# Optimization experiments

Measured on AMD Instinct MI355X. Metric: run time of the kernel, lower is better.

## Reference

```python
import jax, jax.numpy as jnp
import numpy as np
from jax import lax

EPS = 1e-5  # torch LayerNorm / BatchNorm1d default eps
HEADS, DH, DEPTH, C = 4, 128, 2, 512


def setup_inputs() -> dict:
    key = jax.random.key(0)
    ks = iter(jax.random.split(key, 48))
    def rn(shape, scale=1.0):
        return jax.random.normal(next(ks), shape, jnp.float32) * scale
    d, L = 1024, DEPTH
    inp = {}
    inp['x'] = rn((16, 10, 256, d))                      # (b, ncrops, T, d)
    # Temporal embedding: Conv1d(d -> 512, k=3, pad=1) + ReLU
    inp['W_emb'] = rn((C, d, 3), (d * 3) ** -0.5)
    inp['b_emb'] = jnp.zeros((C,), jnp.float32)
    # Transformer (depth=2), params stacked along layer axis
    inp['ln1_g'] = jnp.ones((L, C), jnp.float32); inp['ln1_b'] = jnp.zeros((L, C), jnp.float32)
    inp['W_qkv'] = rn((L, C, 4 * HEADS * DH), C ** -0.5)  # to_qkv (no bias), inner_dim*4 = 2048
    inp['W_o']  = rn((L, 2 * HEADS * DH, C), (2 * HEADS * DH) ** -0.5)
    inp['b_o']  = jnp.zeros((L, C), jnp.float32)
    inp['ln2_g'] = jnp.ones((L, C), jnp.float32); inp['ln2_b'] = jnp.zeros((L, C), jnp.float32)
    inp['W_f1'] = rn((L, C, C), C ** -0.5); inp['b_f1'] = jnp.zeros((L, C), jnp.float32)
    inp['W_f2'] = rn((L, C, C), C ** -0.5); inp['b_f2'] = jnp.zeros((L, C), jnp.float32)
    # NormalHead: conv1 512->32 (k=1), bn1, conv2 32->16 (k=1), bn2, conv3 16->1 (k=1)
    inp['c1_W'] = rn((32, C), C ** -0.5); inp['c1_b'] = jnp.zeros((32,), jnp.float32)
    inp['bn1_g'] = jnp.ones((32,), jnp.float32); inp['bn1_b'] = jnp.zeros((32,), jnp.float32)
    inp['bn1_m'] = rn((32,), 0.1)
    inp['bn1_v'] = jax.random.uniform(next(ks), (32,), jnp.float32, 0.5, 1.5)
    inp['c2_W'] = rn((16, 32), 32 ** -0.5); inp['c2_b'] = jnp.zeros((16,), jnp.float32)
    inp['bn2_g'] = jnp.ones((16,), jnp.float32); inp['bn2_b'] = jnp.zeros((16,), jnp.float32)
    inp['bn2_m'] = rn((16,), 0.1)
    inp['bn2_v'] = jax.random.uniform(next(ks), (16,), jnp.float32, 0.5, 1.5)
    inp['c3_W'] = rn((1, 16), 0.25); inp['c3_b'] = jnp.zeros((1,), jnp.float32)
    return inp


def _ln(z, g, b):
    m = z.mean(-1, keepdims=True)
    v = ((z - m) ** 2).mean(-1, keepdims=True)
    return (z - m) / jnp.sqrt(v + EPS) * g + b


def _bn_eval(z, g, b, m, v):  # z: (B, C, T), eval-mode BatchNorm1d
    return (z - m[None, :, None]) / jnp.sqrt(v[None, :, None] + EPS) * g[None, :, None] + b[None, :, None]


def _k1conv(z, W, b):  # pointwise Conv1d: z (B, Ci, T), W (Co, Ci)
    return jnp.einsum('bct,oc->bot', z, W) + b[None, :, None]


def reference(x, W_emb, b_emb, ln1_g, ln1_b, W_qkv, W_o, b_o, ln2_g, ln2_b,
              W_f1, b_f1, W_f2, b_f2, c1_W, c1_b, bn1_g, bn1_b, bn1_m, bn1_v,
              c2_W, c2_b, bn2_g, bn2_b, bn2_m, bn2_v, c3_W, c3_b):
    b, n, T, d = x.shape
    h = x.reshape(b * n, T, d)
    # Temporal embedding: Conv1d(k=3, pad=1) + ReLU
    h = lax.conv_general_dilated(h.transpose(0, 2, 1), W_emb, (1,), 'SAME',
                                 dimension_numbers=('NCH', 'OIH', 'NCH'))
    h = jax.nn.relu(h + b_emb[None, :, None]).transpose(0, 2, 1)  # (BN, T, 512)

    # fixed positional-decay attention map attn2 (T, T), batch-independent
    idx = jnp.arange(T, dtype=jnp.float32)
    tg = jnp.abs(idx[None, :] - idx[:, None])
    a2 = jnp.exp(-tg / jnp.exp(1.0))
    a2 = a2 / a2.sum(-1)  # NOTE: broadcast over last axis, exactly as in the torch code

    scale = DH ** -0.5
    for l in range(DEPTH):
        z = _ln(h, ln1_g[l], ln1_b[l])
        qkvt = z @ W_qkv[l]                                   # (BN, T, 2048)
        q, k, v, t = jnp.split(qkvt, 4, axis=-1)
        def to_heads(u):
            return u.reshape(u.shape[0], T, HEADS, DH).transpose(0, 2, 1, 3)
        q, k, v, t = map(to_heads, (q, k, v, t))              # (BN, H, T, DH)
        attn1 = jax.nn.softmax(jnp.einsum('bhid,bhjd->bhij', q, k) * scale, axis=-1)
        o1 = jnp.einsum('bhij,bhjd->bhid', attn1, v)
        o2 = jnp.einsum('ij,bhjd->bhid', a2, t)
        o = jnp.concatenate([o1, o2], axis=-1)                # (BN, H, T, 2*DH)
        o = o.transpose(0, 2, 1, 3).reshape(h.shape[0], T, HEADS * 2 * DH)
        h = o @ W_o[l] + b_o[l] + h                           # attn residual
        z = _ln(h, ln2_g[l], ln2_b[l])
        h = (jax.nn.gelu(z @ W_f1[l] + b_f1[l], approximate=False) @ W_f2[l] + b_f2[l]) + h

    # NormalHead on (BN, C, T)
    f = h.transpose(0, 2, 1)
    x1 = _k1conv(f, c1_W, c1_b)                               # (BN, 32, T)
    x2 = _k1conv(jax.nn.relu(_bn_eval(x1, bn1_g, bn1_b, bn1_m, bn1_v)), c2_W, c2_b)  # (BN, 16, T)
    scores = jax.nn.sigmoid(_k1conv(jax.nn.relu(_bn_eval(x2, bn2_g, bn2_b, bn2_m, bn2_v)), c3_W, c3_b))
    normal_scores = scores.reshape(b, n, T).mean(1)           # mean over ncrops -> (b, T)

    def maha(feats, anchor, var):  # Mahalanobis distance vs BN running stats (no eps, as in source)
        dist = jnp.sqrt(jnp.sum((feats - anchor[None, :, None]) ** 2 / var[None, :, None], axis=1))
        return dist.reshape(b, n, T).mean(1)

    distance_sum = maha(x1, bn1_m, bn1_v) + maha(x2, bn2_m, bn2_v)
    return distance_sum * normal_scores                       # (b, T)
```

## Files before the change

### kernel.cpp

```cpp
#include <hip/hip_runtime.h>
#include <math.h>

#define T_    256
#define D_    1024
#define C_    512
#define H_    4
#define DH_   128
#define BNB   160
#define LEPS  1e-5f
#define INV_E 0.36787944117144233f
#define SCALE_ 0.08838834764831845f
#define LDT   40
#define XROW  264192

typedef unsigned short ushort;
typedef unsigned int   uint;
typedef __attribute__((ext_vector_type(8))) short short8;
typedef __attribute__((ext_vector_type(4))) float f32x4;

__device__ __forceinline__ ushort f2b(float f) {
    uint u = __float_as_uint(f);
    u += 0x7fffu + ((u >> 16) & 1u);
    return (ushort)(u >> 16);
}
__device__ __forceinline__ float b2f(ushort u) {
    return __uint_as_float(((uint)u) << 16);
}
__device__ __forceinline__ uint pk(float a, float b) {
    return (uint)f2b(a) | ((uint)f2b(b) << 16);
}
__device__ __forceinline__ void gl2lds(const void* g, void* l) {
    __builtin_amdgcn_global_load_lds(
        (const __attribute__((address_space(1))) void*)g,
        (__attribute__((address_space(3))) void*)l, 16, 0, 0);
}

__global__ void zero_k(float* __restrict__ p, int n) {
    int i = blockIdx.x * 256 + threadIdx.x;
    if (i < n) p[i] = 0.0f;
}

__global__ void xcvt_k(const float* __restrict__ src, ushort* __restrict__ dst, int n4) {
    int i = blockIdx.x * 256 + threadIdx.x;
    if (i < n4) {
        float4 f = ((const float4*)src)[i];
        uint2 v;
        v.x = pk(f.x, f.y);
        v.y = pk(f.z, f.w);
        int e   = i * 4;
        int bn  = e >> 18;
        int rem = e & 262143;
        ((uint2*)(dst + (size_t)bn * XROW + 1024 + rem))[0] = v;
    }
}

__global__ void xpad_k(ushort* __restrict__ dst, int nbn) {
    int i = blockIdx.x * 256 + threadIdx.x;
    if (i >= nbn * 1024) return;
    int bn = i >> 10, j = i & 1023;
    int r = j >> 9, c = j & 511;
    uint* base = (uint*)(dst + (size_t)bn * XROW);
    base[(r ? (XROW - 1024) / 2 : 0) + c] = 0u;
}

__global__ __launch_bounds__(256)
void tconv_k(const float* __restrict__ src, ushort* __restrict__ dst,
             int K, int N) {
    __shared__ float tile[32][33];
    int kb = blockIdx.x * 32, nb = blockIdx.y * 32;
    int tx = threadIdx.x & 31, ty = threadIdx.x >> 5;
#pragma unroll
    for (int i = 0; i < 32; i += 8)
        tile[ty + i][tx] = src[(size_t)(kb + ty + i) * N + nb + tx];
    __syncthreads();
#pragma unroll
    for (int i = 0; i < 32; i += 8)
        dst[(size_t)(nb + ty + i) * K + kb + tx] = f2b(tile[tx][ty + i]);
}

__global__ void bcvt_k(const float* __restrict__ src, ushort* __restrict__ dst, int n) {
    int i = blockIdx.x * 256 + threadIdx.x;
    if (i < n) dst[i] = f2b(src[i]);
}

__global__ void wemb_k(const float* __restrict__ W, ushort* __restrict__ Wt) {
    int idx = blockIdx.x * 256 + threadIdx.x;
    if (idx >= C_ * 3072) return;
    int c = idx / 3072, k = idx % 3072;
    int dt = k >> 10, ci = k & 1023;
    Wt[idx] = f2b(W[(size_t)c * 3072 + ci * 3 + dt]);
}

__global__ void a2_colsum_k(float* __restrict__ s) {
    int j = threadIdx.x;
    float acc = 0.0f;
    for (int k = 0; k < T_; k++) acc += expf(-fabsf((float)(j - k)) * INV_E);
    s[j] = acc;
}

__global__ void a2fill_k(const float* __restrict__ s, ushort* __restrict__ A2) {
    int i = blockIdx.x, j = threadIdx.x;
    A2[i * 256 + j] = f2b(expf(-fabsf((float)(i - j)) * INV_E) / s[j]);
}

__global__ __launch_bounds__(256)
void ln_k(const ushort* __restrict__ X, const float* __restrict__ g,
          const float* __restrict__ b, ushort* __restrict__ Z) {
    int row  = blockIdx.x * 4 + (threadIdx.x >> 6);
    int lane = threadIdx.x & 63;
    const ushort* xr = X + (size_t)row * C_ + lane * 8;
    uint4 raw = *(const uint4*)xr;
    float f[8];
    f[0] = __uint_as_float(raw.x << 16); f[1] = __uint_as_float(raw.x & 0xffff0000u);
    f[2] = __uint_as_float(raw.y << 16); f[3] = __uint_as_float(raw.y & 0xffff0000u);
    f[4] = __uint_as_float(raw.z << 16); f[5] = __uint_as_float(raw.z & 0xffff0000u);
    f[6] = __uint_as_float(raw.w << 16); f[7] = __uint_as_float(raw.w & 0xffff0000u);
    float s = 0.0f, s2 = 0.0f;
#pragma unroll
    for (int u = 0; u < 8; u++) { s += f[u]; s2 += f[u] * f[u]; }
#pragma unroll
    for (int m = 1; m < 64; m <<= 1) {
        s  += __shfl_xor(s, m);
        s2 += __shfl_xor(s2, m);
    }
    float mean = s * (1.0f / C_);
    float var  = s2 * (1.0f / C_) - mean * mean;
    float rinv = rsqrtf(var + LEPS);
    const float* gp = g + lane * 8;
    const float* bp = b + lane * 8;
    float4 g0 = *(const float4*)gp, g1 = *(const float4*)(gp + 4);
    float4 b0 = *(const float4*)bp, b1 = *(const float4*)(bp + 4);
    uint4 outv;
    outv.x = pk((f[0]-mean)*rinv*g0.x+b0.x, (f[1]-mean)*rinv*g0.y+b0.y);
    outv.y = pk((f[2]-mean)*rinv*g0.z+b0.z, (f[3]-mean)*rinv*g0.w+b0.w);
    outv.z = pk((f[4]-mean)*rinv*g1.x+b1.x, (f[5]-mean)*rinv*g1.y+b1.y);
    outv.w = pk((f[6]-mean)*rinv*g1.z+b1.z, (f[7]-mean)*rinv*g1.w+b1.w);
    *(uint4*)(Z + (size_t)row * C_ + lane * 8) = outv;
}


#define VMW_12 asm volatile("s_waitcnt vmcnt(12)" ::: "memory")
#define VMW_10 asm volatile("s_waitcnt vmcnt(10)" ::: "memory")
#define VMW_8  asm volatile("s_waitcnt vmcnt(8)"  ::: "memory")
#define VMW_4  asm volatile("s_waitcnt vmcnt(4)"  ::: "memory")
#define VMW_2  asm volatile("s_waitcnt vmcnt(2)"  ::: "memory")
#define VMW_0  asm volatile("s_waitcnt vmcnt(0)"  ::: "memory")
#define VMW_N
#define BAR() __builtin_amdgcn_s_barrier()
#define LGK4 do { asm volatile("s_waitcnt lgkmcnt(4)" ::: "memory"); \
                  __builtin_amdgcn_sched_barrier(0); } while (0)
#define LGK0 do { asm volatile("s_waitcnt lgkmcnt(0)" ::: "memory"); \
                  __builtin_amdgcn_sched_barrier(0); } while (0)

#define TILE(kt, S, W2, W3, W4, R4) do {                                       \
              \
    _Pragma("unroll") for (int mf = 0; mf < 4; mf++)                           \
      _Pragma("unroll") for (int ks = 0; ks < 2; ks++)                         \
        af[mf][ks] = ldA(kt, mf, ks);                                          \
    _Pragma("unroll") for (int nf = 2; nf < 4; nf++)                           \
      _Pragma("unroll") for (int ks = 0; ks < 2; ks++)                         \
        bf[nf][ks] = ldB(kt, nf, ks);                                          \
    LGK4;                                                                      \
    __builtin_amdgcn_s_setprio(1);                                             \
    _Pragma("unroll") for (int ks = 0; ks < 2; ks++)                           \
      _Pragma("unroll") for (int mf = 0; mf < 4; mf++)                         \
        _Pragma("unroll") for (int nf = 0; nf < 2; nf++)                       \
          acc[mf][nf] = __builtin_amdgcn_mfma_f32_16x16x32_bf16(               \
              af[mf][ks], bf[nf][ks], acc[mf][nf], 0, 0, 0);                   \
    __builtin_amdgcn_s_setprio(0);                                             \
    BAR();                                                                     \
              \
    if (S) { stageA((kt) + 2, 0); stageB((kt) + 2, 0); }                       \
    LGK0;                                                                      \
    __builtin_amdgcn_s_setprio(1);                                             \
    _Pragma("unroll") for (int ks = 0; ks < 2; ks++)                           \
      _Pragma("unroll") for (int mf = 0; mf < 4; mf++)                         \
        _Pragma("unroll") for (int nf = 2; nf < 4; nf++)                       \
          acc[mf][nf] = __builtin_amdgcn_mfma_f32_16x16x32_bf16(               \
              af[mf][ks], bf[nf][ks], acc[mf][nf], 0, 0, 0);                   \
    __builtin_amdgcn_s_setprio(0);                                             \
    VMW_##W2; BAR();                                                           \
       \
    if (S) stageB((kt) + 2, 1);                                                \
    _Pragma("unroll") for (int mf = 0; mf < 4; mf++)                           \
      _Pragma("unroll") for (int ks = 0; ks < 2; ks++)                         \
        af[mf][ks] = ldA(kt, mf + 4, ks);                                      \
    LGK0;                                                                      \
    __builtin_amdgcn_s_setprio(1);                                             \
    _Pragma("unroll") for (int ks = 0; ks < 2; ks++)                           \
      _Pragma("unroll") for (int mf = 0; mf < 4; mf++)                         \
        _Pragma("unroll") for (int nf = 0; nf < 2; nf++)                       \
          acc[mf + 4][nf] = __builtin_amdgcn_mfma_f32_16x16x32_bf16(           \
              af[mf][ks], bf[nf][ks], acc[mf + 4][nf], 0, 0, 0);               \
    __builtin_amdgcn_s_setprio(0);                                             \
    VMW_##W3; BAR();                                                           \
     \
    if (S) stageA((kt) + 2, 1);                                                \
    if (R4)                                                                    \
      _Pragma("unroll") for (int nf = 0; nf < 2; nf++)                         \
        _Pragma("unroll") for (int ks = 0; ks < 2; ks++)                       \
          bf[nf][ks] = ldB((kt) + 1, nf, ks);                                  \
    __builtin_amdgcn_s_setprio(1);                                             \
    _Pragma("unroll") for (int ks = 0; ks < 2; ks++)                           \
      _Pragma("unroll") for (int mf = 0; mf < 4; mf++)                         \
        _Pragma("unroll") for (int nf = 2; nf < 4; nf++)                       \
          acc[mf + 4][nf] = __builtin_amdgcn_mfma_f32_16x16x32_bf16(           \
              af[mf][ks], bf[nf][ks], acc[mf + 4][nf], 0, 0, 0);               \
    __builtin_amdgcn_s_setprio(0);                                             \
    VMW_##W4; BAR();                                                           \
} while (0)

template<int CONV, int ACT, int RESID, int OUTBF>
__global__ __launch_bounds__(512, 2)
void gemm256_k(const ushort* __restrict__ A, const ushort* __restrict__ B,
               const float* __restrict__ bias, const ushort* __restrict__ R,
               void* __restrict__ Cout, int M, int N, int K,
               const ushort* __restrict__ Xp) {
    __shared__ __align__(16) ushort As[32768];
    __shared__ __align__(16) ushort Bs[32768];
    const int tid  = threadIdx.x;
    const int wave = tid >> 6, lane = tid & 63;
    const int wm = wave >> 2, wn = wave & 3;
    const int lm = lane & 15, quad = lane >> 4;

    const int NP = gridDim.x, My = gridDim.y;
    int m_idx, n_idx;
    if ((My & 7) == 0) {
        int bid = blockIdx.y * NP + blockIdx.x;
        m_idx = (bid & 7) + 8 * (bid / (8 * NP));
        n_idx = (bid >> 3) % NP;
    } else {
        m_idx = blockIdx.y; n_idx = blockIdx.x;
    }
    const int m0 = m_idx * 256, n0 = n_idx * 256;

    const int srow = lane >> 3;
    const int scol = ((lane & 7) ^ srow) << 3;

    auto stageA = [&](int kt, int half) {
        ushort* lds = As + (((kt & 1) * 2 + half) << 13) + (wave << 9);
        int r0 = half * 128 + wave * 8 + srow;
        if (CONV) {
            int k0 = kt << 6;
            int dt = k0 >> 10;
            int cb = (k0 & 1023) + scol;
            int g0 = m0 + r0;
            gl2lds(Xp + (size_t)(g0 >> 8) * XROW + ((g0 & 255) + dt) * 1024 + cb, lds);
            int g1 = g0 + 64;
            gl2lds(Xp + (size_t)(g1 >> 8) * XROW + ((g1 & 255) + dt) * 1024 + cb, lds + 4096);
        } else {
            const ushort* ga = A + (size_t)(m0 + r0) * K + (kt << 6) + scol;
            gl2lds(ga, lds);
            gl2lds(ga + (size_t)64 * K, lds + 4096);
        }
    };
    auto stageB = [&](int kt, int half) {
        ushort* lds = Bs + (((kt & 1) * 2 + half) << 13) + (wave << 9);
        const ushort* gb = B + (size_t)(n0 + half * 128 + wave * 8 + srow) * K
                             + (kt << 6) + scol;
        gl2lds(gb, lds);
        gl2lds(gb + (size_t)64 * K, lds + 4096);
    };

    auto ldA = [&](int kt, int mf, int ks) -> short8 {
        int r = wm * 16 + mf * 32 + lm;
        int slot = (quad + ks * 4) ^ (lm & 7);
        return *(const short8*)&As[(((kt & 1) * 2 + (r >> 7)) << 13)
                                   + (r & 127) * 64 + slot * 8];
    };
    auto ldB = [&](int kt, int nf, int ks) -> short8 {
        int r = wn * 16 + nf * 64 + lm;
        int slot = (quad + ks * 4) ^ (lm & 7);
        return *(const short8*)&Bs[(((kt & 1) * 2 + (r >> 7)) << 13)
                                   + (r & 127) * 64 + slot * 8];
    };

    short8 af[4][2], bf[4][2];
    f32x4 acc[8][4];
#pragma unroll
    for (int mf = 0; mf < 8; mf++)
#pragma unroll
        for (int nf = 0; nf < 4; nf++) acc[mf][nf] = (f32x4){0.f, 0.f, 0.f, 0.f};

    const int NT = K >> 6;
    stageA(0, 0); stageB(0, 0); stageB(0, 1); stageA(0, 1);
    stageA(1, 0); stageB(1, 0); stageB(1, 1); stageA(1, 1);
    VMW_10;
    BAR();
#pragma unroll
    for (int nf = 0; nf < 2; nf++)
#pragma unroll
        for (int ks = 0; ks < 2; ks++) bf[nf][ks] = ldB(0, nf, ks);

    for (int kt = 0; kt < NT - 2; kt++)
        TILE(kt, 1, 12, 10, 10, 1);
    TILE(NT - 2, 0, 8, 4, 2, 1);
    TILE(NT - 1, 0, 0, N, N, 0);

#pragma unroll
    for (int mf = 0; mf < 8; mf++) {
        int grow0 = m0 + wm * 16 + mf * 32 + quad * 4;
#pragma unroll
        for (int nf = 0; nf < 4; nf++) {
            int gcol = n0 + wn * 16 + nf * 64 + lm;
            float bia = bias ? bias[gcol] : 0.0f;
            f32x4 v = acc[mf][nf];
#pragma unroll
            for (int i = 0; i < 4; i++) {
                int grow = grow0 + i;
                float val = v[i] + bia;
                if (ACT == 1) val = val * 0.5f * (1.0f + erff(val * 0.70710678118654752f));
                if (ACT == 2) val = fmaxf(val, 0.0f);
                if (RESID) val += b2f(R[(size_t)grow * N + gcol]);
                if (OUTBF) ((ushort*)Cout)[(size_t)grow * N + gcol] = f2b(val);
                else       ((float*)Cout)[(size_t)grow * N + gcol]  = val;
            }
        }
    }
}

template<int CONV, int ACT, int RESID, int OUTBF>
__global__ __launch_bounds__(256)
void gemm_k(const ushort* __restrict__ A, const ushort* __restrict__ B,
            const float* __restrict__ bias, const ushort* __restrict__ R,
            void* __restrict__ Cout, int M, int N, int K,
            const ushort* __restrict__ Xp) {
    __shared__ __align__(16) ushort As[128 * 32];
    __shared__ __align__(16) ushort Bs[128 * 32];
    const int tid  = threadIdx.x;
    const int lane = tid & 63, wave = tid >> 6;
    const int wr = wave >> 1, wc = wave & 1;
    const int lm = lane & 15, quad = lane >> 4;

    const int NP = gridDim.x, My = gridDim.y;
    int m_idx, n_idx;
    if ((My & 7) == 0) {
        int bid = blockIdx.y * NP + blockIdx.x;
        m_idx = (bid & 7) + 8 * (bid / (8 * NP));
        n_idx = (bid >> 3) % NP;
    } else {
        m_idx = blockIdx.y; n_idx = blockIdx.x;
    }
    const int m0 = m_idx * 128, n0 = n_idx * 128;

    const int srow   = lane >> 2;
    const int schunk = (lane & 3) * 8;
    ushort* AsW = As + wave * 32 * 32;
    ushort* BsW = Bs + wave * 32 * 32;

    f32x4 acc[4][4];
#pragma unroll
    for (int mt = 0; mt < 4; mt++)
#pragma unroll
        for (int nt = 0; nt < 4; nt++) acc[mt][nt] = (f32x4){0.f, 0.f, 0.f, 0.f};

    for (int k0 = 0; k0 < K; k0 += 32) {
        if (CONV) {
            int dt = k0 >> 10;
            int ci = (k0 & 1023) + schunk;
            int g0 = m0 + wave * 32 + srow;
            int bn0 = g0 >> 8, t0 = g0 & 255;
            int g1 = g0 + 16;
            int bn1 = g1 >> 8, t1 = g1 & 255;
            gl2lds(Xp + (size_t)bn0 * XROW + (t0 + dt) * 1024 + ci, AsW);
            gl2lds(Xp + (size_t)bn1 * XROW + (t1 + dt) * 1024 + ci, AsW + 16 * 32);
        } else {
            const ushort* ga = A + (size_t)(m0 + wave * 32 + srow) * K + k0 + schunk;
            gl2lds(ga, AsW);
            gl2lds(ga + (size_t)16 * K, AsW + 16 * 32);
        }
        {
            const ushort* gb = B + (size_t)(n0 + wave * 32 + srow) * K + k0 + schunk;
            gl2lds(gb, BsW);
            gl2lds(gb + (size_t)16 * K, BsW + 16 * 32);
        }
        __syncthreads();
        short8 af[4], bfv[4];
#pragma unroll
        for (int mt = 0; mt < 4; mt++)
            af[mt] = *(const short8*)&As[(wr * 64 + mt * 16 + lm) * 32 + quad * 8];
#pragma unroll
        for (int nt = 0; nt < 4; nt++)
            bfv[nt] = *(const short8*)&Bs[(wc * 64 + nt * 16 + lm) * 32 + quad * 8];
#pragma unroll
        for (int mt = 0; mt < 4; mt++)
#pragma unroll
            for (int nt = 0; nt < 4; nt++)
                acc[mt][nt] = __builtin_amdgcn_mfma_f32_16x16x32_bf16(
                    af[mt], bfv[nt], acc[mt][nt], 0, 0, 0);
        __syncthreads();
    }

#pragma unroll
    for (int mt = 0; mt < 4; mt++) {
        int grow0 = m0 + wr * 64 + mt * 16 + quad * 4;
#pragma unroll
        for (int nt = 0; nt < 4; nt++) {
            int gcol = n0 + wc * 64 + nt * 16 + lm;
            float bia = bias ? bias[gcol] : 0.0f;
            f32x4 v = acc[mt][nt];
#pragma unroll
            for (int i = 0; i < 4; i++) {
                int grow = grow0 + i;
                float val = v[i] + bia;
                if (ACT == 1) val = val * 0.5f * (1.0f + erff(val * 0.70710678118654752f));
                if (ACT == 2) val = fmaxf(val, 0.0f);
                if (RESID) val += b2f(R[(size_t)grow * N + gcol]);
                if (OUTBF) ((ushort*)Cout)[(size_t)grow * N + gcol] = f2b(val);
                else       ((float*)Cout)[(size_t)grow * N + gcol]  = val;
            }
        }
    }
}

__global__ __launch_bounds__(256)
void attn1_k(const ushort* __restrict__ qkvt, ushort* __restrict__ O) {
    const int bn = blockIdx.x, h = blockIdx.y;
    const int tid = threadIdx.x;
    const int wave = tid >> 6, lane = tid & 63;
    const int lm = lane & 15, quad = lane >> 4;
    __shared__ __align__(16) ushort Ks[32 * 136];
    __shared__ __align__(16) ushort Vt[128 * 40];
    __shared__ __align__(16) ushort Ps[4][64 * 40];
    const ushort* base = qkvt + (size_t)bn * T_ * 2048;

    short8 aq[4][4];
#pragma unroll
    for (int mt = 0; mt < 4; mt++) {
        const ushort* qrow = base + (size_t)(wave * 64 + mt * 16 + lm) * 2048 + h * DH_;
#pragma unroll
        for (int ks = 0; ks < 4; ks++)
            aq[mt][ks] = *(const short8*)(qrow + ks * 32 + quad * 8);
    }

    f32x4 oacc[4][8];
#pragma unroll
    for (int mt = 0; mt < 4; mt++)
#pragma unroll
        for (int nt = 0; nt < 8; nt++) oacc[mt][nt] = (f32x4){0.f, 0.f, 0.f, 0.f};
    float mrow[4][4], lrow[4][4];
#pragma unroll
    for (int mt = 0; mt < 4; mt++)
#pragma unroll
        for (int i = 0; i < 4; i++) { mrow[mt][i] = -1e30f; lrow[mt][i] = 0.0f; }

    for (int kt = 0; kt < 8; kt++) {
        __syncthreads();
#pragma unroll
        for (int u = 0; u < 2; u++) {
            int ii = tid + u * 256;
            int j = ii >> 4, dc = ii & 15;
            *(uint4*)&Ks[j * 136 + dc * 8] =
                *(const uint4*)(base + (size_t)(kt * 32 + j) * 2048 + 512 + h * DH_ + dc * 8);
        }
        {
            int j = tid & 31, half = tid >> 5;
            const ushort* vrow = base + (size_t)(kt * 32 + j) * 2048 + 1024 + h * DH_ + half * 16;
            uint4 v0 = *(const uint4*)vrow;
            uint4 v1 = *(const uint4*)(vrow + 8);
            ushort e[16];
            *(uint4*)&e[0] = v0; *(uint4*)&e[8] = v1;
#pragma unroll
            for (int u = 0; u < 16; u++)
                Vt[(half * 16 + u) * 40 + j] = e[u];
        }
        __syncthreads();

        f32x4 s[4][2];
#pragma unroll
        for (int mt = 0; mt < 4; mt++)
#pragma unroll
            for (int nt = 0; nt < 2; nt++) s[mt][nt] = (f32x4){0.f, 0.f, 0.f, 0.f};
#pragma unroll
        for (int ks = 0; ks < 4; ks++) {
            short8 bk0 = *(const short8*)&Ks[lm * 136 + ks * 32 + quad * 8];
            short8 bk1 = *(const short8*)&Ks[(16 + lm) * 136 + ks * 32 + quad * 8];
#pragma unroll
            for (int mt = 0; mt < 4; mt++) {
                s[mt][0] = __builtin_amdgcn_mfma_f32_16x16x32_bf16(aq[mt][ks], bk0, s[mt][0], 0, 0, 0);
                s[mt][1] = __builtin_amdgcn_mfma_f32_16x16x32_bf16(aq[mt][ks], bk1, s[mt][1], 0, 0, 0);
            }
        }

#pragma unroll
        for (int mt = 0; mt < 4; mt++) {
#pragma unroll
            for (int i = 0; i < 4; i++) {
                float v0 = s[mt][0][i] * SCALE_;
                float v1 = s[mt][1][i] * SCALE_;
                float rmax = fmaxf(v0, v1);
#pragma unroll
                for (int mk = 1; mk < 16; mk <<= 1)
                    rmax = fmaxf(rmax, __shfl_xor(rmax, mk));
                float mold = mrow[mt][i];
                float mnew = fmaxf(mold, rmax);
                float alpha = __expf(mold - mnew);
                float p0 = __expf(v0 - mnew);
                float p1 = __expf(v1 - mnew);
                float rs = p0 + p1;
#pragma unroll
                for (int mk = 1; mk < 16; mk <<= 1)
                    rs += __shfl_xor(rs, mk);
                lrow[mt][i] = lrow[mt][i] * alpha + rs;
                mrow[mt][i] = mnew;
#pragma unroll
                for (int nt = 0; nt < 8; nt++) {
                    oacc[mt][nt][i] *= alpha;
                }
                int prow = mt * 16 + quad * 4 + i;
                Ps[wave][prow * 40 + lm]      = f2b(p0);
                Ps[wave][prow * 40 + 16 + lm] = f2b(p1);
            }
        }

        short8 ap[4];
#pragma unroll
        for (int mt = 0; mt < 4; mt++)
            ap[mt] = *(const short8*)&Ps[wave][(mt * 16 + lm) * 40 + quad * 8];
#pragma unroll
        for (int nt = 0; nt < 8; nt++) {
            short8 bv = *(const short8*)&Vt[(nt * 16 + lm) * 40 + quad * 8];
#pragma unroll
            for (int mt = 0; mt < 4; mt++)
                oacc[mt][nt] = __builtin_amdgcn_mfma_f32_16x16x32_bf16(ap[mt], bv, oacc[mt][nt], 0, 0, 0);
        }
    }

#pragma unroll
    for (int mt = 0; mt < 4; mt++) {
#pragma unroll
        for (int i = 0; i < 4; i++) {
            int row = wave * 64 + mt * 16 + quad * 4 + i;
            float rinv = 1.0f / lrow[mt][i];
#pragma unroll
            for (int nt = 0; nt < 8; nt++) {
                int d = nt * 16 + lm;
                O[((size_t)bn * T_ + row) * 1024 + h * 256 + d] =
                    f2b(oacc[mt][nt][i] * rinv);
            }
        }
    }
}

__global__ __launch_bounds__(256)
void attn2_k(const ushort* __restrict__ A2, const ushort* __restrict__ qkvt,
             ushort* __restrict__ O) {
    __shared__ __align__(16) ushort As[128 * LDT];
    __shared__ __align__(16) ushort Bs[128 * 48];
    const int tid = threadIdx.x;
    const int bn = blockIdx.z;
    const int m0 = blockIdx.y * 128;
    const int n0 = blockIdx.x * 128;
    const int lane = tid & 63, wave = tid >> 6;
    const int wr = wave >> 1, wc = wave & 1;
    const int lm = lane & 15, quad = lane >> 4;
    const ushort* tbase = qkvt + (size_t)bn * T_ * 2048 + 1536;
    const int r = tid >> 1, c0 = (tid & 1) * 2;

    f32x4 acc[4][4];
#pragma unroll
    for (int mt = 0; mt < 4; mt++)
#pragma unroll
        for (int nt = 0; nt < 4; nt++) acc[mt][nt] = (f32x4){0.f, 0.f, 0.f, 0.f};

    for (int k0 = 0; k0 < 256; k0 += 32) {
        const ushort* Arow = A2 + (size_t)(m0 + r) * 256 + k0;
        *(uint4*)&As[r * LDT + c0 * 8]       = *(const uint4*)(Arow + c0 * 8);
        *(uint4*)&As[r * LDT + (c0 + 1) * 8] = *(const uint4*)(Arow + (c0 + 1) * 8);
        {
            int kr = tid & 31, np = tid >> 5;
            const ushort* trow = tbase + (size_t)(k0 + kr) * 2048 + n0 + np * 16;
            uint4 v0 = *(const uint4*)trow;
            uint4 v1 = *(const uint4*)(trow + 8);
            ushort e[16];
            *(uint4*)&e[0] = v0; *(uint4*)&e[8] = v1;
#pragma unroll
            for (int u = 0; u < 16; u++)
                Bs[(np * 16 + u) * 48 + kr] = e[u];
        }
        __syncthreads();
        short8 af[4], bf[4];
#pragma unroll
        for (int mt = 0; mt < 4; mt++)
            af[mt] = *(const short8*)&As[(wr * 64 + mt * 16 + lm) * LDT + quad * 8];
#pragma unroll
        for (int nt = 0; nt < 4; nt++)
            bf[nt] = *(const short8*)&Bs[(wc * 64 + nt * 16 + lm) * 48 + quad * 8];
#pragma unroll
        for (int mt = 0; mt < 4; mt++)
#pragma unroll
            for (int nt = 0; nt < 4; nt++)
                acc[mt][nt] = __builtin_amdgcn_mfma_f32_16x16x32_bf16(
                    af[mt], bf[nt], acc[mt][nt], 0, 0, 0);
        __syncthreads();
    }

#pragma unroll
    for (int mt = 0; mt < 4; mt++) {
        int row0 = m0 + wr * 64 + mt * 16 + quad * 4;
#pragma unroll
        for (int nt = 0; nt < 4; nt++) {
            int n = n0 + wc * 64 + nt * 16 + lm;
            int h = n >> 7, d = n & 127;
#pragma unroll
            for (int i = 0; i < 4; i++) {
                int row = row0 + i;
                O[((size_t)bn * T_ + row) * 1024 + h * 256 + 128 + d] =
                    f2b(acc[mt][nt][i]);
            }
        }
    }
}

#define BLD 520
__global__ __launch_bounds__(256)
void head1_k(const ushort* __restrict__ Hb, const ushort* __restrict__ c1Wb,
             const float* __restrict__ c1b, float* __restrict__ X1) {
    __shared__ __align__(16) ushort As[128 * LDT];
    __shared__ __align__(16) ushort Bs[32 * BLD];
    const int tid = threadIdx.x;
    const int lane = tid & 63, wave = tid >> 6;
    const int lm = lane & 15, quad = lane >> 4;
    const int m0 = blockIdx.x * 128;
#pragma unroll
    for (int u = 0; u < 8; u++) {
        int ii = tid + u * 256;
        int nrow = ii >> 6;
        int koff = (ii & 63) * 8;
        *(uint4*)&Bs[nrow * BLD + koff] = *(const uint4*)(c1Wb + nrow * 512 + koff);
    }
    f32x4 acc[2][2];
#pragma unroll
    for (int mt = 0; mt < 2; mt++)
#pragma unroll
        for (int nt = 0; nt < 2; nt++) acc[mt][nt] = (f32x4){0.f, 0.f, 0.f, 0.f};

    const int r = tid >> 1, half = tid & 1;
    for (int k0 = 0; k0 < 512; k0 += 32) {
        const ushort* s = Hb + (size_t)(m0 + r) * 512 + k0 + half * 16;
        uint4 v0 = *(const uint4*)s;
        uint4 v1 = *(const uint4*)(s + 8);
        __syncthreads();
        *(uint4*)&As[r * LDT + half * 16]     = v0;
        *(uint4*)&As[r * LDT + half * 16 + 8] = v1;
        __syncthreads();
        short8 af[2], bf[2];
#pragma unroll
        for (int mt = 0; mt < 2; mt++)
            af[mt] = *(const short8*)&As[(wave * 32 + mt * 16 + lm) * LDT + quad * 8];
#pragma unroll
        for (int nt = 0; nt < 2; nt++)
            bf[nt] = *(const short8*)&Bs[(nt * 16 + lm) * BLD + k0 + quad * 8];
#pragma unroll
        for (int mt = 0; mt < 2; mt++)
#pragma unroll
            for (int nt = 0; nt < 2; nt++)
                acc[mt][nt] = __builtin_amdgcn_mfma_f32_16x16x32_bf16(
                    af[mt], bf[nt], acc[mt][nt], 0, 0, 0);
    }
#pragma unroll
    for (int mt = 0; mt < 2; mt++) {
        int row0 = m0 + wave * 32 + mt * 16 + quad * 4;
#pragma unroll
        for (int nt = 0; nt < 2; nt++) {
            int col = nt * 16 + lm;
            float bia = c1b[col];
#pragma unroll
            for (int i = 0; i < 4; i++)
                X1[(size_t)(row0 + i) * 32 + col] = acc[mt][nt][i] + bia;
        }
    }
}

__global__ __launch_bounds__(256)
void head2_k(const float* __restrict__ X1, int bn_base, int M,
             const float* __restrict__ g1, const float* __restrict__ b1,
             const float* __restrict__ m1, const float* __restrict__ v1,
             const float* __restrict__ c2W, const float* __restrict__ c2b,
             const float* __restrict__ g2, const float* __restrict__ b2,
             const float* __restrict__ m2, const float* __restrict__ v2,
             const float* __restrict__ c3W, const float* __restrict__ c3b,
             float* __restrict__ sum_dist, float* __restrict__ sum_score) {
    int row = blockIdx.x * 256 + threadIdx.x;
    if (row >= M) return;
    float x1[32], y1[32];
    const float* xr = X1 + (size_t)row * 32;
#pragma unroll
    for (int c = 0; c < 32; c++) x1[c] = xr[c];
    float d1 = 0.0f;
#pragma unroll
    for (int c = 0; c < 32; c++) {
        float dd = x1[c] - m1[c];
        d1 += dd * dd / v1[c];
        y1[c] = fmaxf(0.0f, dd * rsqrtf(v1[c] + LEPS) * g1[c] + b1[c]);
    }
    float d2 = 0.0f, sc = c3b[0];
#pragma unroll
    for (int o = 0; o < 16; o++) {
        float acc = c2b[o];
        const float* wr = c2W + o * 32;
#pragma unroll
        for (int c = 0; c < 32; c++) acc += wr[c] * y1[c];
        float dd = acc - m2[o];
        d2 += dd * dd / v2[o];
        float y2 = fmaxf(0.0f, dd * rsqrtf(v2[o] + LEPS) * g2[o] + b2[o]);
        sc += c3W[o] * y2;
    }
    float dist = sqrtf(d1) + sqrtf(d2);
    sc = 1.0f / (1.0f + expf(-sc));
    int bn = bn_base + (row >> 8);
    int t = row & 255;
    int b = bn / 10;
    atomicAdd(&sum_dist[b * T_ + t], dist);
    atomicAdd(&sum_score[b * T_ + t], sc);
}

__global__ void combine_k(const float* __restrict__ sd, const float* __restrict__ ss,
                          float* __restrict__ out) {
    int i = blockIdx.x * 256 + threadIdx.x;
    if (i < 16 * T_) out[i] = (sd[i] * 0.1f) * (ss[i] * 0.1f);
}

extern "C" void kernel_launch(void* const* d_in, const int* in_sizes, int n_in,
                              void* d_out, int out_size, void* d_ws, size_t ws_size,
                              hipStream_t stream) {
    const float* x     = (const float*)d_in[0];
    const float* W_emb = (const float*)d_in[1];
    const float* b_emb = (const float*)d_in[2];
    const float* ln1_g = (const float*)d_in[3];
    const float* ln1_b = (const float*)d_in[4];
    const float* W_qkv = (const float*)d_in[5];
    const float* W_o   = (const float*)d_in[6];
    const float* b_o   = (const float*)d_in[7];
    const float* ln2_g = (const float*)d_in[8];
    const float* ln2_b = (const float*)d_in[9];
    const float* W_f1  = (const float*)d_in[10];
    const float* b_f1  = (const float*)d_in[11];
    const float* W_f2  = (const float*)d_in[12];
    const float* b_f2  = (const float*)d_in[13];
    const float* c1_W  = (const float*)d_in[14];
    const float* c1_b  = (const float*)d_in[15];
    const float* bn1_g = (const float*)d_in[16];
    const float* bn1_b = (const float*)d_in[17];
    const float* bn1_m = (const float*)d_in[18];
    const float* bn1_v = (const float*)d_in[19];
    const float* c2_W  = (const float*)d_in[20];
    const float* c2_b  = (const float*)d_in[21];
    const float* bn2_g = (const float*)d_in[22];
    const float* bn2_b = (const float*)d_in[23];
    const float* bn2_m = (const float*)d_in[24];
    const float* bn2_v = (const float*)d_in[25];
    const float* c3_W  = (const float*)d_in[26];
    const float* c3_b  = (const float*)d_in[27];
    float* out = (float*)d_out;

    char* p = (char*)d_ws;
    auto alloc = [&](size_t bytes) -> char* {
        char* q = p; p += (bytes + 255) & ~(size_t)255; return q;
    };
    ushort* wEmb = (ushort*)alloc((size_t)C_ * 3072 * 2);
    ushort* wQkv = (ushort*)alloc((size_t)2 * 2048 * 512 * 2);
    ushort* wO   = (ushort*)alloc((size_t)2 * 512 * 1024 * 2);
    ushort* wF1  = (ushort*)alloc((size_t)2 * 512 * 512 * 2);
    ushort* wF2  = (ushort*)alloc((size_t)2 * 512 * 512 * 2);
    ushort* A2bf = (ushort*)alloc((size_t)256 * 256 * 2);
    ushort* c1Wb = (ushort*)alloc((size_t)32 * 512 * 2);
    float*  s256      = (float*)alloc(256 * 4);
    float*  sum_dist  = (float*)alloc(4096 * 4);
    float*  sum_score = (float*)alloc(4096 * 4);
    size_t fixedB = (size_t)(p - (char*)d_ws);

    int CH = 8;
    const int cands[7] = {160, 80, 40, 32, 20, 16, 10};
    for (int ci = 0; ci < 7; ci++) {
        size_t per = (size_t)cands[ci] * 256 * 10384 + 16384;
        if (fixedB + per <= ws_size) { CH = cands[ci]; break; }
    }
    const int MR = CH * 256;
    ushort* xbp  = (ushort*)alloc((size_t)CH * XROW * 2);
    ushort* h    = (ushort*)alloc((size_t)MR * 512 * 2);
    ushort* z    = (ushort*)alloc((size_t)MR * 512 * 2);
    ushort* qkvt = (ushort*)alloc((size_t)MR * 2048 * 2);
    ushort* o    = (ushort*)alloc((size_t)MR * 1024 * 2);
    ushort* g    = o;
    float*  X1   = (float*)alloc((size_t)MR * 32 * 4);

    zero_k<<<(8192 + 255) / 256, 256, 0, stream>>>(sum_dist, 8192);
    a2_colsum_k<<<1, 256, 0, stream>>>(s256);
    a2fill_k<<<256, 256, 0, stream>>>(s256, A2bf);
    wemb_k<<<(C_ * 3072 + 255) / 256, 256, 0, stream>>>(W_emb, wEmb);
    bcvt_k<<<(32 * 512 + 255) / 256, 256, 0, stream>>>(c1_W, c1Wb, 32 * 512);
    for (int l = 0; l < 2; l++) {
        tconv_k<<<dim3(512 / 32, 2048 / 32), 256, 0, stream>>>(
            W_qkv + (size_t)l * 512 * 2048, wQkv + (size_t)l * 2048 * 512, 512, 2048);
        tconv_k<<<dim3(1024 / 32, 512 / 32), 256, 0, stream>>>(
            W_o + (size_t)l * 1024 * 512, wO + (size_t)l * 512 * 1024, 1024, 512);
        tconv_k<<<dim3(512 / 32, 512 / 32), 256, 0, stream>>>(
            W_f1 + (size_t)l * 512 * 512, wF1 + (size_t)l * 512 * 512, 512, 512);
        tconv_k<<<dim3(512 / 32, 512 / 32), 256, 0, stream>>>(
            W_f2 + (size_t)l * 512 * 512, wF2 + (size_t)l * 512 * 512, 512, 512);
    }

    for (int cs = 0; cs < BNB; cs += CH) {
        const float* xc = x + (size_t)cs * T_ * D_;

        int n4 = MR * 1024 / 4;
        xcvt_k<<<(n4 + 255) / 256, 256, 0, stream>>>(xc, xbp, n4);
        xpad_k<<<(CH * 1024 + 255) / 256, 256, 0, stream>>>(xbp, CH);

        gemm256_k<1, 2, 0, 1><<<dim3(512 / 256, MR / 256), 512, 0, stream>>>(
            nullptr, wEmb, b_emb, nullptr, h, MR, 512, 3072, xbp);

        for (int l = 0; l < 2; l++) {
            ln_k<<<MR / 4, 256, 0, stream>>>(h, ln1_g + l * C_, ln1_b + l * C_, z);
            gemm256_k<0, 0, 0, 1><<<dim3(2048 / 256, MR / 256), 512, 0, stream>>>(
                z, wQkv + (size_t)l * 2048 * 512, nullptr, nullptr, qkvt,
                MR, 2048, 512, nullptr);
            attn1_k<<<dim3(CH, H_), 256, 0, stream>>>(qkvt, o);
            attn2_k<<<dim3(4, 2, CH), 256, 0, stream>>>(A2bf, qkvt, o);
            gemm_k<0, 0, 1, 1><<<dim3(512 / 128, MR / 128), 256, 0, stream>>>(
                o, wO + (size_t)l * 512 * 1024, b_o + l * C_, h, h,
                MR, 512, 1024, nullptr);
            ln_k<<<MR / 4, 256, 0, stream>>>(h, ln2_g + l * C_, ln2_b + l * C_, z);
            gemm_k<0, 1, 0, 1><<<dim3(512 / 128, MR / 128), 256, 0, stream>>>(
                z, wF1 + (size_t)l * 512 * 512, b_f1 + l * C_, nullptr, g,
                MR, 512, 512, nullptr);
            gemm_k<0, 0, 1, 1><<<dim3(512 / 128, MR / 128), 256, 0, stream>>>(
                g, wF2 + (size_t)l * 512 * 512, b_f2 + l * C_, h, h,
                MR, 512, 512, nullptr);
        }

        head1_k<<<MR / 128, 256, 0, stream>>>(h, c1Wb, c1_b, X1);
        head2_k<<<MR / 256, 256, 0, stream>>>(
            X1, cs, MR, bn1_g, bn1_b, bn1_m, bn1_v,
            c2_W, c2_b, bn2_g, bn2_b, bn2_m, bn2_v, c3_W, c3_b,
            sum_dist, sum_score);
    }

    combine_k<<<16, 256, 0, stream>>>(sum_dist, sum_score, out);
}
```

Measured before the change: 1.763 ms.

## Restructure GEMM k-loop prefetch schedule to stage half-tiles one step ahead

Reworks the 256x256 GEMM main-loop pipeline. Global-to-LDS staging of A/B half-tiles is now spread across the four MFMA phases, with parts of tile kt+1 staged during tile kt and parts of kt+2 later. B fragments are reloaded per phase instead of being carried across tiles. This aims to balance memory issue and waits across phases and reduce stalls, but it adds barriers and tighter vmcnt waits, which could serialize more.

```diff
diff --git a/kernel.cpp b/kernel.cpp
--- a/kernel.cpp
+++ b/kernel.cpp
@@ -139,28 +139,25 @@
 }
 
 
-#define VMW_12 asm volatile("s_waitcnt vmcnt(12)" ::: "memory")
-#define VMW_10 asm volatile("s_waitcnt vmcnt(10)" ::: "memory")
-#define VMW_8  asm volatile("s_waitcnt vmcnt(8)"  ::: "memory")
-#define VMW_4  asm volatile("s_waitcnt vmcnt(4)"  ::: "memory")
-#define VMW_2  asm volatile("s_waitcnt vmcnt(2)"  ::: "memory")
-#define VMW_0  asm volatile("s_waitcnt vmcnt(0)"  ::: "memory")
+#define VMW_8 asm volatile("s_waitcnt vmcnt(8)" ::: "memory")
+#define VMW_4 asm volatile("s_waitcnt vmcnt(4)" ::: "memory")
+#define VMW_2 asm volatile("s_waitcnt vmcnt(2)" ::: "memory")
+#define VMW_0 asm volatile("s_waitcnt vmcnt(0)" ::: "memory")
 #define VMW_N
 #define BAR() __builtin_amdgcn_s_barrier()
-#define LGK4 do { asm volatile("s_waitcnt lgkmcnt(4)" ::: "memory"); \
-                  __builtin_amdgcn_sched_barrier(0); } while (0)
-#define LGK0 do { asm volatile("s_waitcnt lgkmcnt(0)" ::: "memory"); \
-                  __builtin_amdgcn_sched_barrier(0); } while (0)
-
-#define TILE(kt, S, W2, W3, W4, R4) do {                                       \
-              \
+#define LGK0() do { asm volatile("s_waitcnt lgkmcnt(0)" ::: "memory"); \
+                    __builtin_amdgcn_sched_barrier(0); } while (0)
+
+#define TILE(kt, S1, S2, S3, S4, W1, W2, W4) do {                              \
+                               \
     _Pragma("unroll") for (int mf = 0; mf < 4; mf++)                           \
       _Pragma("unroll") for (int ks = 0; ks < 2; ks++)                         \
         af[mf][ks] = ldA(kt, mf, ks);                                          \
-    _Pragma("unroll") for (int nf = 2; nf < 4; nf++)                           \
+    _Pragma("unroll") for (int nf = 0; nf < 2; nf++)                           \
       _Pragma("unroll") for (int ks = 0; ks < 2; ks++)                         \
         bf[nf][ks] = ldB(kt, nf, ks);                                          \
-    LGK4;                                                                      \
+    if (S1) stageB((kt) + 1, 1);                                               \
+    VMW_##W1; BAR(); LGK0();                                                   \
     __builtin_amdgcn_s_setprio(1);                                             \
     _Pragma("unroll") for (int ks = 0; ks < 2; ks++)                           \
       _Pragma("unroll") for (int mf = 0; mf < 4; mf++)                         \
@@ -169,9 +166,12 @@
               af[mf][ks], bf[nf][ks], acc[mf][nf], 0, 0, 0);                   \
     __builtin_amdgcn_s_setprio(0);                                             \
     BAR();                                                                     \
-              \
-    if (S) { stageA((kt) + 2, 0); stageB((kt) + 2, 0); }                       \
-    LGK0;                                                                      \
+                \
+    _Pragma("unroll") for (int nf = 2; nf < 4; nf++)                           \
+      _Pragma("unroll") for (int ks = 0; ks < 2; ks++)                         \
+        bf[nf][ks] = ldB(kt, nf, ks);                                          \
+    if (S2) stageA((kt) + 1, 1);                                               \
+    VMW_##W2; BAR(); LGK0();                                                   \
     __builtin_amdgcn_s_setprio(1);                                             \
     _Pragma("unroll") for (int ks = 0; ks < 2; ks++)                           \
       _Pragma("unroll") for (int mf = 0; mf < 4; mf++)                         \
@@ -179,13 +179,13 @@
           acc[mf][nf] = __builtin_amdgcn_mfma_f32_16x16x32_bf16(               \
               af[mf][ks], bf[nf][ks], acc[mf][nf], 0, 0, 0);                   \
     __builtin_amdgcn_s_setprio(0);                                             \
-    VMW_##W2; BAR();                                                           \
-       \
-    if (S) stageB((kt) + 2, 1);                                                \
+    BAR();                                                                     \
+                               \
     _Pragma("unroll") for (int mf = 0; mf < 4; mf++)                           \
       _Pragma("unroll") for (int ks = 0; ks < 2; ks++)                         \
         af[mf][ks] = ldA(kt, mf + 4, ks);                                      \
-    LGK0;                                                                      \
+    if (S3) stageA((kt) + 2, 0);                                               \
+    BAR(); LGK0();                                                             \
     __builtin_amdgcn_s_setprio(1);                                             \
     _Pragma("unroll") for (int ks = 0; ks < 2; ks++)                           \
       _Pragma("unroll") for (int mf = 0; mf < 4; mf++)                         \
@@ -193,13 +193,10 @@
           acc[mf + 4][nf] = __builtin_amdgcn_mfma_f32_16x16x32_bf16(           \
               af[mf][ks], bf[nf][ks], acc[mf + 4][nf], 0, 0, 0);               \
     __builtin_amdgcn_s_setprio(0);                                             \
-    VMW_##W3; BAR();                                                           \
-     \
-    if (S) stageA((kt) + 2, 1);                                                \
-    if (R4)                                                                    \
-      _Pragma("unroll") for (int nf = 0; nf < 2; nf++)                         \
-        _Pragma("unroll") for (int ks = 0; ks < 2; ks++)                       \
-          bf[nf][ks] = ldB((kt) + 1, nf, ks);                                  \
+    BAR();                                                                     \
+              \
+    if (S4) stageB((kt) + 2, 0);                                               \
+    VMW_##W4; BAR();                                                           \
     __builtin_amdgcn_s_setprio(1);                                             \
     _Pragma("unroll") for (int ks = 0; ks < 2; ks++)                           \
       _Pragma("unroll") for (int mf = 0; mf < 4; mf++)                         \
@@ -207,7 +204,7 @@
           acc[mf + 4][nf] = __builtin_amdgcn_mfma_f32_16x16x32_bf16(           \
               af[mf][ks], bf[nf][ks], acc[mf + 4][nf], 0, 0, 0);               \
     __builtin_amdgcn_s_setprio(0);                                             \
-    VMW_##W4; BAR();                                                           \
+    BAR();                                                                     \
 } while (0)
 
 template<int CONV, int ACT, int RESID, int OUTBF>
@@ -284,18 +281,14 @@
 
     const int NT = K >> 6;
     stageA(0, 0); stageB(0, 0); stageB(0, 1); stageA(0, 1);
-    stageA(1, 0); stageB(1, 0); stageB(1, 1); stageA(1, 1);
-    VMW_10;
+    stageA(1, 0); stageB(1, 0);
+    VMW_8;
     BAR();
-#pragma unroll
-    for (int nf = 0; nf < 2; nf++)
-#pragma unroll
-        for (int ks = 0; ks < 2; ks++) bf[nf][ks] = ldB(0, nf, ks);
 
     for (int kt = 0; kt < NT - 2; kt++)
-        TILE(kt, 1, 12, 10, 10, 1);
-    TILE(NT - 2, 0, 8, 4, 2, 1);
-    TILE(NT - 1, 0, 0, N, N, 0);
+        TILE(kt, 1, 1, 1, 1, 8, 8, 8);
+    TILE(NT - 2, 1, 1, 0, 0, 8, 8, 4);
+    TILE(NT - 1, 0, 0, 0, 0, 2, 0, N);
 
 #pragma unroll
     for (int mf = 0; mf < 8; mf++) {
```

Measured after the change: 1.559 ms. -11.6%, faster.
